# Optimization experiments

Measured on AMD Instinct MI355X. Metric: run time of the kernel, lower is better.

## Reference

```python
import jax, jax.numpy as jnp
import numpy as np

D_MODEL = 512
NHEAD = 8
D_K = D_MODEL // NHEAD


def setup_inputs() -> dict:
    key = jax.random.key(0)
    ks = jax.random.split(key, 9)
    s = 1.0 / np.sqrt(D_MODEL)
    x = jax.random.normal(ks[0], (2, 2048, D_MODEL), dtype=jnp.float32)
    # torch Linear weights: [out_features, in_features]
    Wq = jax.random.uniform(ks[1], (D_MODEL, D_MODEL), jnp.float32, -s, s)
    bq = jax.random.uniform(ks[2], (D_MODEL,), jnp.float32, -s, s)
    Wk = jax.random.uniform(ks[3], (D_MODEL, D_MODEL), jnp.float32, -s, s)
    bk = jax.random.uniform(ks[4], (D_MODEL,), jnp.float32, -s, s)
    Wv = jax.random.uniform(ks[5], (D_MODEL, D_MODEL), jnp.float32, -s, s)
    bv = jax.random.uniform(ks[6], (D_MODEL,), jnp.float32, -s, s)
    Wo = jax.random.uniform(ks[7], (D_MODEL, D_MODEL), jnp.float32, -s, s)
    bo = jax.random.uniform(ks[8], (D_MODEL,), jnp.float32, -s, s)
    return {"x": x, "Wq": Wq, "bq": bq, "Wk": Wk, "bk": bk,
            "Wv": Wv, "bv": bv, "Wo": Wo, "bo": bo}


def reference(x, Wq, bq, Wk, bk, Wv, bv, Wo, bo):
    B, S, D = x.shape
    H, Dk = NHEAD, D_K

    def proj(W, b):
        # torch Linear: x @ W.T + b -> [B, S, D] -> [B, H, S, Dk]
        y = jnp.einsum('bsd,ed->bse', x, W) + b
        return y.reshape(B, S, H, Dk).transpose(0, 2, 1, 3)

    q = proj(Wq, bq)
    k = proj(Wk, bk)
    v = proj(Wv, bv)

    scores = jnp.einsum('bhqd,bhkd->bhqk', q, k) / jnp.sqrt(jnp.float32(Dk))
    attn = jax.nn.softmax(scores, axis=-1)  # explicit O(S^2) attention matrix
    out = jnp.einsum('bhqk,bhkd->bhqd', attn, v)
    out = out.transpose(0, 2, 1, 3).reshape(B, S, D)
    return jnp.einsum('bsd,ed->bse', out, Wo) + bo
```

## Files before the change

### kernel.cpp

```cpp
#include <hip/hip_runtime.h>

typedef __bf16 bf16_t;
typedef bf16_t bf16x8 __attribute__((ext_vector_type(8)));
typedef bf16_t bf16x4 __attribute__((ext_vector_type(4)));
typedef float  floatx4 __attribute__((ext_vector_type(4)));

#define D_MODEL 512
#define NHEAD   8
#define DK      64
#define BATCH   2
#define SEQ     2048
#define MTOT    (BATCH*SEQ)
#define QSCALE  0.18033688011112042591f

static __device__ __forceinline__ floatx4 mfma16(bf16x8 a, bf16x8 b, floatx4 c) {
    return __builtin_amdgcn_mfma_f32_16x16x32_bf16(a, b, c, 0, 0, 0);
}

static __device__ __forceinline__ void glds16(bf16_t* lds, const bf16_t* g) {
    __builtin_amdgcn_global_load_lds(
        (const __attribute__((address_space(1))) unsigned int*)g,
        (__attribute__((address_space(3))) unsigned int*)lds,
        16, 0, 0);
}

__global__ __launch_bounds__(256)
void to_bf16(const float* __restrict__ x,
             const float* __restrict__ Wq, const float* __restrict__ Wk,
             const float* __restrict__ Wv, const float* __restrict__ Wo,
             bf16_t* __restrict__ xb, bf16_t* __restrict__ wqb,
             bf16_t* __restrict__ wkb, bf16_t* __restrict__ wvb,
             bf16_t* __restrict__ wob)
{
    const int blk = blockIdx.x;
    const float* src; bf16_t* dst; size_t base;
    if      (blk < 1024) { src = x;  dst = xb;  base = (size_t)blk * 2048; }
    else if (blk < 1152) { src = Wq; dst = wqb; base = (size_t)(blk - 1024) * 2048; }
    else if (blk < 1280) { src = Wk; dst = wkb; base = (size_t)(blk - 1152) * 2048; }
    else if (blk < 1408) { src = Wv; dst = wvb; base = (size_t)(blk - 1280) * 2048; }
    else                 { src = Wo; dst = wob; base = (size_t)(blk - 1408) * 2048; }
    const size_t off = base + (size_t)threadIdx.x * 8;
    const float4 a = *(const float4*)(src + off);
    const float4 b = *(const float4*)(src + off + 4);
    bf16x8 p;
    p[0]=(bf16_t)a.x; p[1]=(bf16_t)a.y; p[2]=(bf16_t)a.z; p[3]=(bf16_t)a.w;
    p[4]=(bf16_t)b.x; p[5]=(bf16_t)b.y; p[6]=(bf16_t)b.z; p[7]=(bf16_t)b.w;
    *(bf16x8*)(dst + off) = p;
}

__global__ __launch_bounds__(256)
void qkv_proj(const bf16_t* __restrict__ xb,
              const bf16_t* __restrict__ wqb, const float* __restrict__ bq,
              const bf16_t* __restrict__ wkb, const float* __restrict__ bk,
              const bf16_t* __restrict__ wvb, const float* __restrict__ bv,
              bf16_t* __restrict__ q_ws, bf16_t* __restrict__ k_ws,
              bf16_t* __restrict__ vt_ws)
{
    __shared__ bf16_t As[128 * 32];
    __shared__ bf16_t Bs[128 * 32];

    const int mtile = blockIdx.x;
    const int ntile = blockIdx.y;
    const int which = ntile >> 2;
    const int nsub  = ntile & 3;
    const bf16_t* W   = (which == 0) ? wqb : (which == 1) ? wkb : wvb;
    const float* bias = (which == 0) ? bq  : (which == 1) ? bk  : bv;

    const int tid  = threadIdx.x;
    const int lane = tid & 63;
    const int wave = tid >> 6;
    const int wm = wave & 1, wn = wave >> 1;
    const int l15 = lane & 15, quad = lane >> 4;
    const int m0 = mtile * 128;
    const int n0 = nsub * 128;
    const int lr = lane >> 2;
    const int lc = (lane & 3) * 8;

    floatx4 acc[4][4] = {};

    for (int k0 = 0; k0 < 512; k0 += 32) {
        __syncthreads();
        #pragma unroll
        for (int q = 0; q < 2; ++q) {
            const int r = wave * 32 + q * 16;
            glds16(&As[r * 32], xb + (size_t)(m0 + r + lr) * 512 + k0 + lc);
            glds16(&Bs[r * 32], W  + (size_t)(n0 + r + lr) * 512 + k0 + lc);
        }
        __syncthreads();

        bf16x8 af[4], bfr[4];
        #pragma unroll
        for (int i = 0; i < 4; ++i)
            af[i] = *(const bf16x8*)(&As[(wm * 64 + i * 16 + l15) * 32 + quad * 8]);
        #pragma unroll
        for (int j = 0; j < 4; ++j)
            bfr[j] = *(const bf16x8*)(&Bs[(wn * 64 + j * 16 + l15) * 32 + quad * 8]);
        #pragma unroll
        for (int i = 0; i < 4; ++i)
            #pragma unroll
            for (int j = 0; j < 4; ++j)
                acc[i][j] = mfma16(af[i], bfr[j], acc[i][j]);
    }

    const float scale = (which == 0) ? QSCALE : 1.0f;
    #pragma unroll
    for (int j = 0; j < 4; ++j) {
        const int e = n0 + wn * 64 + j * 16 + l15;
        const float be = bias[e];
        const int h = e >> 6, d = e & 63;
        #pragma unroll
        for (int i = 0; i < 4; ++i) {
            const int mbase = m0 + wm * 64 + i * 16 + quad * 4;
            const int b = mbase >> 11;
            const int sl = mbase & 2047;
            floatx4 c = acc[i][j];
            if (which == 2) {
                bf16x4 pk;
                #pragma unroll
                for (int r = 0; r < 4; ++r) pk[r] = (bf16_t)(c[r] + be);
                *(bf16x4*)(vt_ws + ((size_t)((b * 8 + h) * 64 + d)) * 2048 + sl) = pk;
            } else {
                bf16_t* dst = (which == 0) ? q_ws : k_ws;
                #pragma unroll
                for (int r = 0; r < 4; ++r)
                    dst[(size_t)(b * 8 + h) * (SEQ * DK) + (size_t)(sl + r) * 64 + d] =
                        (bf16_t)((c[r] + be) * scale);
            }
        }
    }
}

#define PS 68
__global__ __launch_bounds__(256, 3)
void attn_kernel(const bf16_t* __restrict__ q_ws, const bf16_t* __restrict__ k_ws,
                 const bf16_t* __restrict__ vt_ws, bf16_t* __restrict__ attn_ws)
{
    __shared__ bf16_t KV[2][2][2][64 * 32];
    __shared__ bf16_t Ps [4][32 * PS];

    const int bh = blockIdx.x;
    const int qt = blockIdx.y;
    const int tid = threadIdx.x, lane = tid & 63, wave = tid >> 6;
    const int l15 = lane & 15, quad = lane >> 4;
    const int g  = wave >> 1;
    const int wq = wave & 1;
    const int lr = lane >> 2, lc = (lane & 3) * 8;

    const bf16_t* Qb  = q_ws  + (size_t)bh * SEQ * DK;
    const bf16_t* Kb  = k_ws  + (size_t)bh * SEQ * DK;
    const bf16_t* Vtb = vt_ws + (size_t)bh * DK * SEQ;
    bf16_t* Pw = &Ps[wave][0];

    bf16x8 aq[2][2];
    #pragma unroll
    for (int mt = 0; mt < 2; ++mt)
        #pragma unroll
        for (int c = 0; c < 2; ++c)
            aq[mt][c] = *(const bf16x8*)(Qb +
                (size_t)(qt * 64 + wq * 32 + mt * 16 + l15) * 64 + c * 32 + quad * 8);

    floatx4 O[2][4] = {};
    float rs[2][4] = {};

    for (int t = 0; t < 16; ++t) {
        __syncthreads();
        {
            const int r0 = wave * 16;
            const int kg0 = t * 128, kg1 = t * 128 + 64;
            glds16(&KV[0][0][0][r0 * 32], Kb + (size_t)(kg0 + r0 + lr) * 64 + lc);
            glds16(&KV[0][0][1][r0 * 32], Kb + (size_t)(kg0 + r0 + lr) * 64 + 32 + lc);
            glds16(&KV[0][1][0][r0 * 32], Kb + (size_t)(kg1 + r0 + lr) * 64 + lc);
            glds16(&KV[0][1][1][r0 * 32], Kb + (size_t)(kg1 + r0 + lr) * 64 + 32 + lc);
            glds16(&KV[1][0][0][r0 * 32], Vtb + (size_t)(r0 + lr) * 2048 + kg0 + lc);
            glds16(&KV[1][0][1][r0 * 32], Vtb + (size_t)(r0 + lr) * 2048 + kg0 + 32 + lc);
            glds16(&KV[1][1][0][r0 * 32], Vtb + (size_t)(r0 + lr) * 2048 + kg1 + lc);
            glds16(&KV[1][1][1][r0 * 32], Vtb + (size_t)(r0 + lr) * 2048 + kg1 + 32 + lc);
        }
        __syncthreads();

        floatx4 sc[2][4];
        #pragma unroll
        for (int kf = 0; kf < 4; ++kf) {
            bf16x8 b0 = *(const bf16x8*)(&KV[0][g][0][(kf * 16 + l15) * 32 + quad * 8]);
            bf16x8 b1 = *(const bf16x8*)(&KV[0][g][1][(kf * 16 + l15) * 32 + quad * 8]);
            #pragma unroll
            for (int mt = 0; mt < 2; ++mt) {
                floatx4 z = {0.f, 0.f, 0.f, 0.f};
                z = mfma16(aq[mt][0], b0, z);
                z = mfma16(aq[mt][1], b1, z);
                sc[mt][kf] = z;
            }
        }

        #pragma unroll
        for (int mt = 0; mt < 2; ++mt)
            #pragma unroll
            for (int kf = 0; kf < 4; ++kf)
                #pragma unroll
                for (int r = 0; r < 4; ++r) {
                    const float p = __builtin_amdgcn_exp2f(sc[mt][kf][r]);
                    rs[mt][r] += p;
                    Pw[(mt * 16 + quad * 4 + r) * PS + kf * 16 + l15] = (bf16_t)p;
                }
        asm volatile("s_waitcnt lgkmcnt(0)" ::: "memory");

        bf16x8 ap[2][2];
        #pragma unroll
        for (int mt = 0; mt < 2; ++mt) {
            bf16x4 p0 = *(const bf16x4*)(&Pw[(mt * 16 + l15) * PS + quad * 8]);
            bf16x4 p1 = *(const bf16x4*)(&Pw[(mt * 16 + l15) * PS + quad * 8 + 4]);
            bf16x4 p2 = *(const bf16x4*)(&Pw[(mt * 16 + l15) * PS + 32 + quad * 8]);
            bf16x4 p3 = *(const bf16x4*)(&Pw[(mt * 16 + l15) * PS + 32 + quad * 8 + 4]);
            ap[mt][0] = __builtin_shufflevector(p0, p1, 0, 1, 2, 3, 4, 5, 6, 7);
            ap[mt][1] = __builtin_shufflevector(p2, p3, 0, 1, 2, 3, 4, 5, 6, 7);
        }

        #pragma unroll
        for (int df = 0; df < 4; ++df) {
            bf16x8 b0 = *(const bf16x8*)(&KV[1][g][0][(df * 16 + l15) * 32 + quad * 8]);
            bf16x8 b1 = *(const bf16x8*)(&KV[1][g][1][(df * 16 + l15) * 32 + quad * 8]);
            #pragma unroll
            for (int mt = 0; mt < 2; ++mt) {
                O[mt][df] = mfma16(ap[mt][0], b0, O[mt][df]);
                O[mt][df] = mfma16(ap[mt][1], b1, O[mt][df]);
            }
        }
    }

    float* scratch = (float*)&KV[0][0][0][0];
    __syncthreads();
    if (g == 1) {
        float* s = scratch + (size_t)(wq * 64 + lane) * 41;
        #pragma unroll
        for (int mt = 0; mt < 2; ++mt) {
            #pragma unroll
            for (int df = 0; df < 4; ++df)
                #pragma unroll
                for (int r = 0; r < 4; ++r) s[mt * 16 + df * 4 + r] = O[mt][df][r];
            #pragma unroll
            for (int r = 0; r < 4; ++r) s[32 + mt * 4 + r] = rs[mt][r];
        }
    }
    __syncthreads();
    if (g == 0) {
        const float* s = scratch + (size_t)(wq * 64 + lane) * 41;
        #pragma unroll
        for (int mt = 0; mt < 2; ++mt) {
            #pragma unroll
            for (int df = 0; df < 4; ++df)
                #pragma unroll
                for (int r = 0; r < 4; ++r) O[mt][df][r] += s[mt * 16 + df * 4 + r];
            #pragma unroll
            for (int r = 0; r < 4; ++r) rs[mt][r] += s[32 + mt * 4 + r];
        }

        #pragma unroll
        for (int off = 1; off < 16; off <<= 1)
            #pragma unroll
            for (int mt = 0; mt < 2; ++mt)
                #pragma unroll
                for (int r = 0; r < 4; ++r) rs[mt][r] += __shfl_xor(rs[mt][r], off, 64);

        const int b = bh >> 3, h = bh & 7;
        #pragma unroll
        for (int mt = 0; mt < 2; ++mt)
            #pragma unroll
            for (int r = 0; r < 4; ++r) {
                const float rinv = 1.0f / rs[mt][r];
                const int s_ = qt * 64 + wq * 32 + mt * 16 + quad * 4 + r;
                const size_t base = ((size_t)b * 2048 + s_) * 512 + h * 64;
                #pragma unroll
                for (int df = 0; df < 4; ++df)
                    attn_ws[base + df * 16 + l15] = (bf16_t)(O[mt][df][r] * rinv);
            }
    }
}

__global__ __launch_bounds__(256)
void out_proj(const bf16_t* __restrict__ attn_ws, const bf16_t* __restrict__ wob,
              const float* __restrict__ bo, float* __restrict__ y)
{
    __shared__ bf16_t As[64 * 32];
    __shared__ bf16_t Bs[128 * 32];

    const int mtile = blockIdx.x;
    const int ntile = blockIdx.y;
    const int tid = threadIdx.x, lane = tid & 63, wave = tid >> 6;
    const int wm = wave & 1, wn = wave >> 1;
    const int l15 = lane & 15, quad = lane >> 4;
    const int m0 = mtile * 64;
    const int n0 = ntile * 128;
    const int lr = lane >> 2, lc = (lane & 3) * 8;

    floatx4 acc[2][4] = {};

    for (int k0 = 0; k0 < 512; k0 += 32) {
        __syncthreads();
        glds16(&As[wave * 16 * 32], attn_ws + (size_t)(m0 + wave * 16 + lr) * 512 + k0 + lc);
        #pragma unroll
        for (int q = 0; q < 2; ++q) {
            const int r = wave * 32 + q * 16;
            glds16(&Bs[r * 32], wob + (size_t)(n0 + r + lr) * 512 + k0 + lc);
        }
        __syncthreads();

        bf16x8 af[2], bfr[4];
        #pragma unroll
        for (int i = 0; i < 2; ++i)
            af[i] = *(const bf16x8*)(&As[(wm * 32 + i * 16 + l15) * 32 + quad * 8]);
        #pragma unroll
        for (int j = 0; j < 4; ++j)
            bfr[j] = *(const bf16x8*)(&Bs[(wn * 64 + j * 16 + l15) * 32 + quad * 8]);
        #pragma unroll
        for (int i = 0; i < 2; ++i)
            #pragma unroll
            for (int j = 0; j < 4; ++j)
                acc[i][j] = mfma16(af[i], bfr[j], acc[i][j]);
    }

    #pragma unroll
    for (int j = 0; j < 4; ++j) {
        const int e = n0 + wn * 64 + j * 16 + l15;
        const float be = bo[e];
        #pragma unroll
        for (int i = 0; i < 2; ++i) {
            const int mb = m0 + wm * 32 + i * 16 + quad * 4;
            #pragma unroll
            for (int r = 0; r < 4; ++r)
                y[(size_t)(mb + r) * 512 + e] = acc[i][j][r] + be;
        }
    }
}

extern "C" void kernel_launch(void* const* d_in, const int* in_sizes, int n_in,
                              void* d_out, int out_size, void* d_ws, size_t ws_size,
                              hipStream_t stream) {
    (void)in_sizes; (void)n_in; (void)out_size; (void)ws_size;
    const float* x  = (const float*)d_in[0];
    const float* Wq = (const float*)d_in[1];
    const float* bq = (const float*)d_in[2];
    const float* Wk = (const float*)d_in[3];
    const float* bk = (const float*)d_in[4];
    const float* Wv = (const float*)d_in[5];
    const float* bv = (const float*)d_in[6];
    const float* Wo = (const float*)d_in[7];
    const float* bo = (const float*)d_in[8];

    bf16_t* xb   = (bf16_t*)d_ws;
    bf16_t* wqb  = xb   + (size_t)MTOT * D_MODEL;
    bf16_t* wkb  = wqb  + (size_t)D_MODEL * D_MODEL;
    bf16_t* wvb  = wkb  + (size_t)D_MODEL * D_MODEL;
    bf16_t* wob  = wvb  + (size_t)D_MODEL * D_MODEL;
    bf16_t* qws  = wob  + (size_t)D_MODEL * D_MODEL;
    bf16_t* kws  = qws  + (size_t)MTOT * D_MODEL;
    bf16_t* vtws = kws  + (size_t)MTOT * D_MODEL;
    bf16_t* aws  = vtws + (size_t)MTOT * D_MODEL;

    to_bf16    <<<1536, 256, 0, stream>>>(x, Wq, Wk, Wv, Wo, xb, wqb, wkb, wvb, wob);
    qkv_proj   <<<dim3(32, 12), 256, 0, stream>>>(xb, wqb, bq, wkb, bk, wvb, bv, qws, kws, vtws);
    attn_kernel<<<dim3(16, 32), 256, 0, stream>>>(qws, kws, vtws, aws);
    out_proj   <<<dim3(64, 4),  256, 0, stream>>>(aws, wob, bo, (float*)d_out);
}
```

Baseline: 137.6 us.

## Swizzle global layouts for conflict-free LDS and keep P in registers via transposed QK^T

Global tensors (x, weights, K, V^T, attention output) are now written in XOR-swizzled column orders so that the direct global-to-LDS loads land in bank-conflict-free positions, and the readers un-swizzle on access. The attention kernel computes S^T = K·Q^T so each lane's score fragment can be fed straight into a 16x16x16 bf16 MFMA for P·V. This removes the per-wave LDS round trip for P and frees shared memory to raise occupancy to 4 blocks. Row-sum reduction is reorganised around the new fragment layout. The cost is more index arithmetic and scattered global writes in the producers, plus correctness that depends on every producer and consumer agreeing on the swizzle.

```diff
diff --git a/kernel.cpp b/kernel.cpp
--- a/kernel.cpp
+++ b/kernel.cpp
@@ -4,6 +4,7 @@
 typedef bf16_t bf16x8 __attribute__((ext_vector_type(8)));
 typedef bf16_t bf16x4 __attribute__((ext_vector_type(4)));
 typedef float  floatx4 __attribute__((ext_vector_type(4)));
+typedef short  s16x4   __attribute__((ext_vector_type(4)));
 
 #define D_MODEL 512
 #define NHEAD   8
@@ -15,6 +16,9 @@
 
 static __device__ __forceinline__ floatx4 mfma16(bf16x8 a, bf16x8 b, floatx4 c) {
     return __builtin_amdgcn_mfma_f32_16x16x32_bf16(a, b, c, 0, 0, 0);
+}
+static __device__ __forceinline__ floatx4 mfma16k16(s16x4 a, s16x4 b, floatx4 c) {
+    return __builtin_amdgcn_mfma_f32_16x16x16bf16_1k(a, b, c, 0, 0, 0);
 }
 
 static __device__ __forceinline__ void glds16(bf16_t* lds, const bf16_t* g) {
@@ -45,7 +49,8 @@
     bf16x8 p;
     p[0]=(bf16_t)a.x; p[1]=(bf16_t)a.y; p[2]=(bf16_t)a.z; p[3]=(bf16_t)a.w;
     p[4]=(bf16_t)b.x; p[5]=(bf16_t)b.y; p[6]=(bf16_t)b.z; p[7]=(bf16_t)b.w;
-    *(bf16x8*)(dst + off) = p;
+    const size_t off2 = off ^ ((((off >> 10) & 3)) << 3);
+    *(bf16x8*)(dst + off2) = p;
 }
 
 __global__ __launch_bounds__(256)
@@ -75,6 +80,7 @@
     const int n0 = nsub * 128;
     const int lr = lane >> 2;
     const int lc = (lane & 3) * 8;
+    const int csw = (quad ^ ((l15 >> 1) & 3)) * 8;
 
     floatx4 acc[4][4] = {};
 
@@ -91,10 +97,10 @@
         bf16x8 af[4], bfr[4];
         #pragma unroll
         for (int i = 0; i < 4; ++i)
-            af[i] = *(const bf16x8*)(&As[(wm * 64 + i * 16 + l15) * 32 + quad * 8]);
+            af[i] = *(const bf16x8*)(&As[(wm * 64 + i * 16 + l15) * 32 + csw]);
         #pragma unroll
         for (int j = 0; j < 4; ++j)
-            bfr[j] = *(const bf16x8*)(&Bs[(wn * 64 + j * 16 + l15) * 32 + quad * 8]);
+            bfr[j] = *(const bf16x8*)(&Bs[(wn * 64 + j * 16 + l15) * 32 + csw]);
         #pragma unroll
         for (int i = 0; i < 4; ++i)
             #pragma unroll
@@ -102,7 +108,6 @@
                 acc[i][j] = mfma16(af[i], bfr[j], acc[i][j]);
     }
 
-    const float scale = (which == 0) ? QSCALE : 1.0f;
     #pragma unroll
     for (int j = 0; j < 4; ++j) {
         const int e = n0 + wn * 64 + j * 16 + l15;
@@ -118,25 +123,32 @@
                 bf16x4 pk;
                 #pragma unroll
                 for (int r = 0; r < 4; ++r) pk[r] = (bf16_t)(c[r] + be);
-                *(bf16x4*)(vt_ws + ((size_t)((b * 8 + h) * 64 + d)) * 2048 + sl) = pk;
+                const int slz = (sl & ~63) | ((((sl >> 3) & 7) ^ (d & 7)) << 3) | (sl & 7);
+                *(bf16x4*)(vt_ws + ((size_t)((b * 8 + h) * 64 + d)) * 2048 + slz) = pk;
+            } else if (which == 1) {
+                #pragma unroll
+                for (int r = 0; r < 4; ++r) {
+                    const int s = sl + r;
+                    const int dz = ((((d >> 3) ^ (s & 7))) << 3) | (d & 7);
+                    k_ws[(size_t)(b * 8 + h) * (SEQ * DK) + (size_t)s * 64 + dz] =
+                        (bf16_t)(c[r] + be);
+                }
             } else {
-                bf16_t* dst = (which == 0) ? q_ws : k_ws;
                 #pragma unroll
                 for (int r = 0; r < 4; ++r)
-                    dst[(size_t)(b * 8 + h) * (SEQ * DK) + (size_t)(sl + r) * 64 + d] =
-                        (bf16_t)((c[r] + be) * scale);
-            }
-        }
-    }
-}
-
-#define PS 68
-__global__ __launch_bounds__(256, 3)
+                    q_ws[(size_t)(b * 8 + h) * (SEQ * DK) + (size_t)(sl + r) * 64 + d] =
+                        (bf16_t)((c[r] + be) * QSCALE);
+            }
+        }
+    }
+}
+
+__global__ __launch_bounds__(256, 4)
 void attn_kernel(const bf16_t* __restrict__ q_ws, const bf16_t* __restrict__ k_ws,
                  const bf16_t* __restrict__ vt_ws, bf16_t* __restrict__ attn_ws)
 {
-    __shared__ bf16_t KV[2][2][2][64 * 32];
-    __shared__ bf16_t Ps [4][32 * PS];
+    __shared__ bf16_t Kt[2][64 * 64];
+    __shared__ bf16_t Vt[2][64 * 64];
 
     const int bh = blockIdx.x;
     const int qt = blockIdx.y;
@@ -144,12 +156,15 @@
     const int l15 = lane & 15, quad = lane >> 4;
     const int g  = wave >> 1;
     const int wq = wave & 1;
-    const int lr = lane >> 2, lc = (lane & 3) * 8;
 
     const bf16_t* Qb  = q_ws  + (size_t)bh * SEQ * DK;
     const bf16_t* Kb  = k_ws  + (size_t)bh * SEQ * DK;
     const bf16_t* Vtb = vt_ws + (size_t)bh * DK * SEQ;
-    bf16_t* Pw = &Ps[wave][0];
+
+    const int sp = wave & 1;
+    bf16_t* stile = (wave < 2) ? &Kt[sp][0] : &Vt[sp][0];
+    const int srow8 = lane >> 3;
+    const int scol  = (lane & 7) * 8;
 
     bf16x8 aq[2][2];
     #pragma unroll
@@ -160,118 +175,111 @@
                 (size_t)(qt * 64 + wq * 32 + mt * 16 + l15) * 64 + c * 32 + quad * 8);
 
     floatx4 O[2][4] = {};
-    float rs[2][4] = {};
+    float rs[2] = {0.f, 0.f};
+    const int ksw0 = ((0 + quad) ^ (l15 & 7)) * 8;
+    const int ksw1 = ((4 + quad) ^ (l15 & 7)) * 8;
 
     for (int t = 0; t < 16; ++t) {
         __syncthreads();
         {
-            const int r0 = wave * 16;
-            const int kg0 = t * 128, kg1 = t * 128 + 64;
-            glds16(&KV[0][0][0][r0 * 32], Kb + (size_t)(kg0 + r0 + lr) * 64 + lc);
-            glds16(&KV[0][0][1][r0 * 32], Kb + (size_t)(kg0 + r0 + lr) * 64 + 32 + lc);
-            glds16(&KV[0][1][0][r0 * 32], Kb + (size_t)(kg1 + r0 + lr) * 64 + lc);
-            glds16(&KV[0][1][1][r0 * 32], Kb + (size_t)(kg1 + r0 + lr) * 64 + 32 + lc);
-            glds16(&KV[1][0][0][r0 * 32], Vtb + (size_t)(r0 + lr) * 2048 + kg0 + lc);
-            glds16(&KV[1][0][1][r0 * 32], Vtb + (size_t)(r0 + lr) * 2048 + kg0 + 32 + lc);
-            glds16(&KV[1][1][0][r0 * 32], Vtb + (size_t)(r0 + lr) * 2048 + kg1 + lc);
-            glds16(&KV[1][1][1][r0 * 32], Vtb + (size_t)(r0 + lr) * 2048 + kg1 + 32 + lc);
-        }
-        __syncthreads();
-
-        floatx4 sc[2][4];
+            const int kg = t * 128 + sp * 64;
+            if (wave < 2) {
+                #pragma unroll
+                for (int i = 0; i < 8; ++i)
+                    glds16(stile + i * 512,
+                           Kb + (size_t)(kg + i * 8 + srow8) * 64 + scol);
+            } else {
+                #pragma unroll
+                for (int i = 0; i < 8; ++i)
+                    glds16(stile + i * 512,
+                           Vtb + (size_t)(i * 8 + srow8) * 2048 + kg + scol);
+            }
+        }
+        __syncthreads();
+
+        s16x4 pf[2][4];
         #pragma unroll
         for (int kf = 0; kf < 4; ++kf) {
-            bf16x8 b0 = *(const bf16x8*)(&KV[0][g][0][(kf * 16 + l15) * 32 + quad * 8]);
-            bf16x8 b1 = *(const bf16x8*)(&KV[0][g][1][(kf * 16 + l15) * 32 + quad * 8]);
+            const bf16_t* krow = &Kt[g][(kf * 16 + l15) * 64];
+            bf16x8 k0 = *(const bf16x8*)(krow + ksw0);
+            bf16x8 k1 = *(const bf16x8*)(krow + ksw1);
             #pragma unroll
             for (int mt = 0; mt < 2; ++mt) {
                 floatx4 z = {0.f, 0.f, 0.f, 0.f};
-                z = mfma16(aq[mt][0], b0, z);
-                z = mfma16(aq[mt][1], b1, z);
-                sc[mt][kf] = z;
-            }
-        }
-
-        #pragma unroll
-        for (int mt = 0; mt < 2; ++mt)
-            #pragma unroll
-            for (int kf = 0; kf < 4; ++kf)
+                z = mfma16(k0, aq[mt][0], z);
+                z = mfma16(k1, aq[mt][1], z);
+                bf16x4 pk;
+                float s = 0.f;
                 #pragma unroll
                 for (int r = 0; r < 4; ++r) {
-                    const float p = __builtin_amdgcn_exp2f(sc[mt][kf][r]);
-                    rs[mt][r] += p;
-                    Pw[(mt * 16 + quad * 4 + r) * PS + kf * 16 + l15] = (bf16_t)p;
+                    const float p = __builtin_amdgcn_exp2f(z[r]);
+                    s += p;
+                    pk[r] = (bf16_t)p;
                 }
-        asm volatile("s_waitcnt lgkmcnt(0)" ::: "memory");
-
-        bf16x8 ap[2][2];
-        #pragma unroll
-        for (int mt = 0; mt < 2; ++mt) {
-            bf16x4 p0 = *(const bf16x4*)(&Pw[(mt * 16 + l15) * PS + quad * 8]);
-            bf16x4 p1 = *(const bf16x4*)(&Pw[(mt * 16 + l15) * PS + quad * 8 + 4]);
-            bf16x4 p2 = *(const bf16x4*)(&Pw[(mt * 16 + l15) * PS + 32 + quad * 8]);
-            bf16x4 p3 = *(const bf16x4*)(&Pw[(mt * 16 + l15) * PS + 32 + quad * 8 + 4]);
-            ap[mt][0] = __builtin_shufflevector(p0, p1, 0, 1, 2, 3, 4, 5, 6, 7);
-            ap[mt][1] = __builtin_shufflevector(p2, p3, 0, 1, 2, 3, 4, 5, 6, 7);
-        }
-
-        #pragma unroll
-        for (int df = 0; df < 4; ++df) {
-            bf16x8 b0 = *(const bf16x8*)(&KV[1][g][0][(df * 16 + l15) * 32 + quad * 8]);
-            bf16x8 b1 = *(const bf16x8*)(&KV[1][g][1][(df * 16 + l15) * 32 + quad * 8]);
-            #pragma unroll
-            for (int mt = 0; mt < 2; ++mt) {
-                O[mt][df] = mfma16(ap[mt][0], b0, O[mt][df]);
-                O[mt][df] = mfma16(ap[mt][1], b1, O[mt][df]);
-            }
-        }
-    }
-
-    float* scratch = (float*)&KV[0][0][0][0];
+                rs[mt] += s;
+                pf[mt][kf] = __builtin_bit_cast(s16x4, pk);
+            }
+        }
+
+        #pragma unroll
+        for (int kg = 0; kg < 4; ++kg) {
+            const int voff = (((kg * 2 + (quad >> 1)) ^ (l15 & 7)) * 8) + (quad & 1) * 4;
+            #pragma unroll
+            for (int df = 0; df < 4; ++df) {
+                const s16x4 v = *(const s16x4*)(&Vt[g][(df * 16 + l15) * 64 + voff]);
+                #pragma unroll
+                for (int mt = 0; mt < 2; ++mt)
+                    O[mt][df] = mfma16k16(pf[mt][kg], v, O[mt][df]);
+            }
+        }
+    }
+
+    #pragma unroll
+    for (int mt = 0; mt < 2; ++mt) {
+        rs[mt] += __shfl_xor(rs[mt], 16, 64);
+        rs[mt] += __shfl_xor(rs[mt], 32, 64);
+    }
+
+    float* scratch = (float*)&Kt[0][0];
     __syncthreads();
     if (g == 1) {
-        float* s = scratch + (size_t)(wq * 64 + lane) * 41;
+        float* s = scratch + (size_t)(wq * 64 + lane) * 35;
         #pragma unroll
         for (int mt = 0; mt < 2; ++mt) {
             #pragma unroll
             for (int df = 0; df < 4; ++df)
                 #pragma unroll
                 for (int r = 0; r < 4; ++r) s[mt * 16 + df * 4 + r] = O[mt][df][r];
-            #pragma unroll
-            for (int r = 0; r < 4; ++r) s[32 + mt * 4 + r] = rs[mt][r];
+            s[32 + mt] = rs[mt];
         }
     }
     __syncthreads();
     if (g == 0) {
-        const float* s = scratch + (size_t)(wq * 64 + lane) * 41;
+        const float* s = scratch + (size_t)(wq * 64 + lane) * 35;
         #pragma unroll
         for (int mt = 0; mt < 2; ++mt) {
             #pragma unroll
             for (int df = 0; df < 4; ++df)
                 #pragma unroll
                 for (int r = 0; r < 4; ++r) O[mt][df][r] += s[mt * 16 + df * 4 + r];
-            #pragma unroll
-            for (int r = 0; r < 4; ++r) rs[mt][r] += s[32 + mt * 4 + r];
-        }
-
-        #pragma unroll
-        for (int off = 1; off < 16; off <<= 1)
-            #pragma unroll
-            for (int mt = 0; mt < 2; ++mt)
-                #pragma unroll
-                for (int r = 0; r < 4; ++r) rs[mt][r] += __shfl_xor(rs[mt][r], off, 64);
+            rs[mt] += s[32 + mt];
+        }
 
         const int b = bh >> 3, h = bh & 7;
         #pragma unroll
         for (int mt = 0; mt < 2; ++mt)
             #pragma unroll
             for (int r = 0; r < 4; ++r) {
-                const float rinv = 1.0f / rs[mt][r];
+                const float rv = __shfl(rs[mt], (quad << 4) + ((quad & 3) << 2) + r, 64);
+                const float rinv = 1.0f / rv;
                 const int s_ = qt * 64 + wq * 32 + mt * 16 + quad * 4 + r;
-                const size_t base = ((size_t)b * 2048 + s_) * 512 + h * 64;
-                #pragma unroll
-                for (int df = 0; df < 4; ++df)
-                    attn_ws[base + df * 16 + l15] = (bf16_t)(O[mt][df][r] * rinv);
+                const int sw = ((s_ >> 1) & 3) << 3;
+                const size_t base = ((size_t)b * 2048 + s_) * 512;
+                #pragma unroll
+                for (int df = 0; df < 4; ++df) {
+                    const int col = h * 64 + df * 16 + l15;
+                    attn_ws[base + (col ^ sw)] = (bf16_t)(O[mt][df][r] * rinv);
+                }
             }
     }
 }
@@ -291,6 +299,7 @@
     const int m0 = mtile * 64;
     const int n0 = ntile * 128;
     const int lr = lane >> 2, lc = (lane & 3) * 8;
+    const int csw = (quad ^ ((l15 >> 1) & 3)) * 8;
 
     floatx4 acc[2][4] = {};
 
@@ -307,10 +316,10 @@
         bf16x8 af[2], bfr[4];
         #pragma unroll
         for (int i = 0; i < 2; ++i)
-            af[i] = *(const bf16x8*)(&As[(wm * 32 + i * 16 + l15) * 32 + quad * 8]);
+            af[i] = *(const bf16x8*)(&As[(wm * 32 + i * 16 + l15) * 32 + csw]);
         #pragma unroll
         for (int j = 0; j < 4; ++j)
-            bfr[j] = *(const bf16x8*)(&Bs[(wn * 64 + j * 16 + l15) * 32 + quad * 8]);
+            bfr[j] = *(const bf16x8*)(&Bs[(wn * 64 + j * 16 + l15) * 32 + csw]);
         #pragma unroll
         for (int i = 0; i < 2; ++i)
             #pragma unroll
```

After: 131.8 us. -4.3%, faster.
